# Kernel tuning notes

Hardware: AMD Instinct MI355X
Metric: run time of the kernel (lower is better)

## Reference

```python
import jax, jax.numpy as jnp
import numpy as np

H = 16  # num_heads
EPS = 1e-12  # F.normalize eps


def setup_inputs() -> dict:
    key = jax.random.key(0)
    ks = jax.random.split(key, 7)
    B, L, D = 2, 2048, 1024
    s = 0.02  # small init scale for numerical sanity
    return {
        "x": jax.random.normal(ks[0], (B, L, D), dtype=jnp.float32),
        "Wq": jax.random.normal(ks[1], (D, D), dtype=jnp.float32) * s,
        "Wk": jax.random.normal(ks[2], (D, D), dtype=jnp.float32) * s,
        "Wv": jax.random.normal(ks[3], (D, D), dtype=jnp.float32) * s,
        "Wo": jax.random.normal(ks[4], (D, D), dtype=jnp.float32) * s,
        "Wb": jax.random.normal(ks[5], (D, H), dtype=jnp.float32) * s,
        "bb": jnp.zeros((H,), dtype=jnp.float32),
    }


def _l2norm(t):
    # matches torch F.normalize(p=2, dim=-1): x / max(||x||, eps)
    n = jnp.sqrt(jnp.sum(t * t, axis=-1, keepdims=True))
    return t / jnp.maximum(n, EPS)


def reference(x, Wq, Wk, Wv, Wo, Wb, bb):
    B, L, Dm = x.shape
    Dh = Dm // H
    q = (x @ Wq).reshape(B, L, H, Dh)
    k = (x @ Wk).reshape(B, L, H, Dh)
    v = (x @ Wv).reshape(B, L, H, Dh)
    beta = jax.nn.sigmoid(x @ Wb + bb)  # [B, L, H]
    q = _l2norm(q)
    k = _l2norm(k)
    # out[b,l,h,e] = sum_{t<=l} beta[b,t,h] * <q[b,l,h], k[b,t,h]> * v[b,t,h,e]
    # Exact reformulation of the cumsum-of-outer-products in the source,
    # avoiding the B*L*H*Dh*Dh state blow-up.
    scores = jnp.einsum('blhd,bthd->bhlt', q, k)
    scores = scores * beta.transpose(0, 2, 1)[:, :, None, :]  # scale by beta_t
    mask = jnp.tril(jnp.ones((L, L), dtype=scores.dtype))  # causal incl. diagonal
    scores = scores * mask
    out = jnp.einsum('bhlt,bthe->blhe', scores, v).reshape(B, L, Dm)
    return out @ Wo
```

## Files before the change

### kernel.cpp

```cpp
#include <hip/hip_runtime.h>
#include <stdint.h>

#define DEV static __device__ __forceinline__

typedef __bf16 bf16x8 __attribute__((ext_vector_type(8)));
typedef unsigned short u16x8 __attribute__((ext_vector_type(8)));
typedef float f32x4 __attribute__((ext_vector_type(4)));

DEV unsigned short f2bf(float f) {
    unsigned int u = __builtin_bit_cast(unsigned int, f);
    u = (u + 0x7FFFu + ((u >> 16) & 1u)) >> 16;
    return (unsigned short)u;
}
DEV float bf2f(unsigned short h) {
    unsigned int u = ((unsigned int)h) << 16;
    return __builtin_bit_cast(float, u);
}

__global__ __launch_bounds__(256) void k_cvt(const float4* __restrict__ src,
                                             ushort4* __restrict__ dst, int n4) {
    int i = blockIdx.x * 256 + threadIdx.x;
    if (i < n4) {
        float4 v = src[i];
        ushort4 o;
        o.x = f2bf(v.x); o.y = f2bf(v.y); o.z = f2bf(v.z); o.w = f2bf(v.w);
        dst[i] = o;
    }
}

__global__ __launch_bounds__(256) void k_transpose_w(
    const float* __restrict__ Wq, const float* __restrict__ Wk,
    const float* __restrict__ Wv, const float* __restrict__ Wo,
    unsigned short* __restrict__ Wqkvt, unsigned short* __restrict__ Wot) {
    __shared__ float tile[32][33];
    int z = blockIdx.z;
    const float* W = (z == 0) ? Wq : (z == 1) ? Wk : (z == 2) ? Wv : Wo;
    int k0 = blockIdx.x * 32, n0 = blockIdx.y * 32;
    int tx = threadIdx.x, ty = threadIdx.y;
    #pragma unroll
    for (int r = 0; r < 32; r += 8)
        tile[ty + r][tx] = W[(size_t)(k0 + ty + r) * 1024 + n0 + tx];
    __syncthreads();
    #pragma unroll
    for (int r = 0; r < 32; r += 8) {
        float v = tile[tx][ty + r];
        int n = n0 + ty + r, k = k0 + tx;
        if (z < 3) Wqkvt[(size_t)(z * 1024 + n) * 1024 + k] = f2bf(v);
        else       Wot[(size_t)n * 1024 + k] = f2bf(v);
    }
}

__global__ __launch_bounds__(256) void k_beta(const float* __restrict__ x,
                                              const float* __restrict__ Wb,
                                              const float* __restrict__ bb,
                                              float* __restrict__ beta) {
    __shared__ float WbT[16 * 1024];
    int tid = threadIdx.x;
    #pragma unroll
    for (int j = 0; j < 16; j++) {
        int idx4 = tid + 256 * j;
        float4 v = ((const float4*)Wb)[idx4];
        int i = idx4 >> 2;
        int h0 = (idx4 & 3) * 4;
        WbT[(h0 + 0) * 1024 + (i ^ ((h0 + 0) << 2))] = v.x;
        WbT[(h0 + 1) * 1024 + (i ^ ((h0 + 1) << 2))] = v.y;
        WbT[(h0 + 2) * 1024 + (i ^ ((h0 + 2) << 2))] = v.z;
        WbT[(h0 + 3) * 1024 + (i ^ ((h0 + 3) << 2))] = v.w;
    }
    __syncthreads();
    int w = tid >> 6, lane = tid & 63;
    #pragma unroll 1
    for (int r = 0; r < 4; r++) {
        int row = blockIdx.x * 16 + w * 4 + r;
        const float* xr = x + (size_t)row * 1024;
        float acc[16] = {};
        #pragma unroll
        for (int k = 0; k < 16; k++) {
            int i = lane + 64 * k;
            float xv = xr[i];
            #pragma unroll
            for (int h = 0; h < 16; h++)
                acc[h] += xv * WbT[h * 1024 + (i ^ (h << 2))];
        }
        #pragma unroll
        for (int h = 0; h < 16; h++) {
            #pragma unroll
            for (int m = 32; m; m >>= 1) acc[h] += __shfl_xor(acc[h], m, 64);
        }
        if (lane == 0) {
            #pragma unroll
            for (int h = 0; h < 16; h++)
                beta[row * 16 + h] = 1.f / (1.f + __expf(-(acc[h] + bb[h])));
        }
    }
}

__global__ __launch_bounds__(256) void k_norm(unsigned short* __restrict__ qk,
                                              const float* __restrict__ beta) {
    int gid = blockIdx.x * 4 + (threadIdx.x >> 6);
    int lane = threadIdx.x & 63;
    int row = gid >> 4, h = gid & 15;
    unsigned short* p = qk + (size_t)row * 3072 + h * 64;
    float v = bf2f(p[lane]);
    float ss = v * v;
    #pragma unroll
    for (int m = 32; m; m >>= 1) ss += __shfl_xor(ss, m, 64);
    float scale = 1.f / fmaxf(sqrtf(ss), 1e-12f);
    if (beta) scale *= beta[row * 16 + h];
    p[lane] = f2bf(v * scale);
}

template <bool OUT_BF16>
__global__ __launch_bounds__(256) void k_gemm(const unsigned short* __restrict__ A,
                                              const unsigned short* __restrict__ Bt,
                                              void* __restrict__ C, int ldc) {
    __shared__ unsigned short As[128 * 32];
    __shared__ unsigned short Bs[128 * 32];
    int m0 = blockIdx.x * 128, n0 = blockIdx.y * 128;
    int tid = threadIdx.x;
    int w = tid >> 6, lane = tid & 63, g = lane >> 4, ln = lane & 15;
    int wr = w >> 1, wc = w & 1;
    f32x4 acc[4][4] = {};
    for (int k0 = 0; k0 < 1024; k0 += 32) {
        #pragma unroll
        for (int cc = 0; cc < 2; cc++) {
            int c = tid + cc * 256;
            int row = c >> 2, sl = c & 3;
            int ps = (sl + (row >> 1)) & 3;
            uint4 da = *(const uint4*)(A + (size_t)(m0 + row) * 1024 + k0 + sl * 8);
            *(uint4*)(&As[row * 32 + ps * 8]) = da;
            uint4 db = *(const uint4*)(Bt + (size_t)(n0 + row) * 1024 + k0 + sl * 8);
            *(uint4*)(&Bs[row * 32 + ps * 8]) = db;
        }
        __syncthreads();
        bf16x8 af[4], bfr[4];
        #pragma unroll
        for (int mi = 0; mi < 4; mi++) {
            int row = wr * 64 + mi * 16 + ln;
            int ps = (g + (row >> 1)) & 3;
            af[mi] = *(const bf16x8*)(&As[row * 32 + ps * 8]);
        }
        #pragma unroll
        for (int ni = 0; ni < 4; ni++) {
            int row = wc * 64 + ni * 16 + ln;
            int ps = (g + (row >> 1)) & 3;
            bfr[ni] = *(const bf16x8*)(&Bs[row * 32 + ps * 8]);
        }
        #pragma unroll
        for (int mi = 0; mi < 4; mi++)
            #pragma unroll
            for (int ni = 0; ni < 4; ni++)
                acc[mi][ni] = __builtin_amdgcn_mfma_f32_16x16x32_bf16(
                    af[mi], bfr[ni], acc[mi][ni], 0, 0, 0);
        __syncthreads();
    }
    #pragma unroll
    for (int mi = 0; mi < 4; mi++)
        #pragma unroll
        for (int ni = 0; ni < 4; ni++)
            #pragma unroll
            for (int r = 0; r < 4; r++) {
                int row = m0 + wr * 64 + mi * 16 + g * 4 + r;
                int col = n0 + wc * 64 + ni * 16 + ln;
                float v = acc[mi][ni][r];
                if (OUT_BF16) ((unsigned short*)C)[(size_t)row * ldc + col] = f2bf(v);
                else          ((float*)C)[(size_t)row * ldc + col] = v;
            }
}

DEV int vswz(int dh, int ks) { return (ks ^ (dh & 7) ^ ((dh >> 3) & 7)) & 7; }

__global__ __launch_bounds__(256) void k_state(const unsigned short* __restrict__ QKV,
                                               unsigned short* __restrict__ Mbuf) {
    __shared__ unsigned short Kt[64 * 64];
    __shared__ unsigned short Vt[64 * 64];
    int c = blockIdx.x, bh = blockIdx.y;
    int b = bh >> 4, h = bh & 15;
    int tid = threadIdx.x, w = tid >> 6, lane = tid & 63, g = lane >> 4, ln = lane & 15;
    int row0 = b * 2048 + c * 64;
    const unsigned short* Kg = QKV + 1024;
    const unsigned short* Vg = QKV + 2048;
    #pragma unroll
    for (int cc = 0; cc < 2; cc++) {
        int ci = tid + cc * 256;
        int r = ci >> 3, sl = ci & 7;
        uint4 kd = *(const uint4*)(Kg + (size_t)(row0 + r) * 3072 + h * 64 + sl * 8);
        uint4 vd = *(const uint4*)(Vg + (size_t)(row0 + r) * 3072 + h * 64 + sl * 8);
        union { uint4 q; unsigned short s[8]; } uk, uv;
        uk.q = kd; uv.q = vd;
        #pragma unroll
        for (int i = 0; i < 8; i++) {
            int dh = sl * 8 + i;
            int off = dh * 64 + vswz(dh, r >> 3) * 8 + (r & 7);
            Kt[off] = uk.s[i];
            Vt[off] = uv.s[i];
        }
    }
    __syncthreads();
    f32x4 macc[4] = {};
    #pragma unroll
    for (int st = 0; st < 2; st++) {
        int c0 = st * 32 + g * 4;
        int rk = w * 16 + ln;
        uint2 klo = *(const uint2*)(&Kt[rk * 64 + vswz(rk, c0 >> 3) * 8 + (c0 & 7)]);
        uint2 khi = *(const uint2*)(&Kt[rk * 64 + vswz(rk, (c0 + 16) >> 3) * 8 + (c0 & 7)]);
        uint4 kc = make_uint4(klo.x, klo.y, khi.x, khi.y);
        bf16x8 bfrag = __builtin_bit_cast(bf16x8, kc);
        #pragma unroll
        for (int mt = 0; mt < 4; mt++) {
            int rv = mt * 16 + ln;
            uint2 lo = *(const uint2*)(&Vt[rv * 64 + vswz(rv, c0 >> 3) * 8 + (c0 & 7)]);
            uint2 hi = *(const uint2*)(&Vt[rv * 64 + vswz(rv, (c0 + 16) >> 3) * 8 + (c0 & 7)]);
            uint4 comb = make_uint4(lo.x, lo.y, hi.x, hi.y);
            bf16x8 afrag = __builtin_bit_cast(bf16x8, comb);
            macc[mt] = __builtin_amdgcn_mfma_f32_16x16x32_bf16(afrag, bfrag, macc[mt], 0, 0, 0);
        }
    }
    unsigned short* Mc = Mbuf + ((size_t)bh * 32 + c) * 4096;
    #pragma unroll
    for (int mt = 0; mt < 4; mt++)
        #pragma unroll
        for (int r = 0; r < 4; r++)
            Mc[(mt * 16 + g * 4 + r) * 64 + w * 16 + ln] = f2bf(macc[mt][r]);
}

__global__ __launch_bounds__(256) void k_prefix(unsigned short* __restrict__ Mbuf) {
    int bh = blockIdx.x >> 3, slice = blockIdx.x & 7;
    int base = slice * 512 + threadIdx.x * 2;
    unsigned short* M = Mbuf + (size_t)bh * 32 * 4096 + base;
    unsigned int v[32];
    #pragma unroll
    for (int c = 0; c < 32; c++) v[c] = *(const unsigned int*)(M + (size_t)c * 4096);
    float a0 = 0.f, a1 = 0.f;
    #pragma unroll
    for (int c = 0; c < 32; c++) {
        unsigned int pack = (unsigned int)f2bf(a0) | ((unsigned int)f2bf(a1) << 16);
        *(unsigned int*)(M + (size_t)c * 4096) = pack;
        a0 += bf2f((unsigned short)(v[c] & 0xFFFF));
        a1 += bf2f((unsigned short)(v[c] >> 16));
    }
}

__global__ __launch_bounds__(256) void k_attn2(const unsigned short* __restrict__ QKV,
                                               const unsigned short* __restrict__ Sbuf,
                                               unsigned short* __restrict__ attn) {
    __shared__ unsigned short Ks[64 * 64];
    __shared__ unsigned short Vt[64 * 64];
    __shared__ unsigned short STs[64 * 64];
    int qt = blockIdx.x, bh = blockIdx.y;
    int b = bh >> 4, h = bh & 15;
    int tid = threadIdx.x, w = tid >> 6, lane = tid & 63, g = lane >> 4, ln = lane & 15;
    int rowbase = b * 2048 + qt * 64;

    const unsigned short* Qrow = QKV + (size_t)(rowbase + w * 16 + ln) * 3072 + h * 64;
    bf16x8 qf[2];
    qf[0] = *(const bf16x8*)(Qrow + g * 8);
    qf[1] = *(const bf16x8*)(Qrow + 32 + g * 8);

    const unsigned short* Kg = QKV + 1024;
    const unsigned short* Vg = QKV + 2048;
    const unsigned short* Sg = Sbuf + ((size_t)bh * 32 + qt) * 4096;

    #pragma unroll
    for (int cc = 0; cc < 2; cc++) {
        int c = tid + cc * 256;
        int r = c >> 3, sl = c & 7;
        uint4 kd = *(const uint4*)(Kg + (size_t)(rowbase + r) * 3072 + h * 64 + sl * 8);
        *(uint4*)(&Ks[r * 64 + ((sl ^ (r & 7)) * 8)]) = kd;
        uint4 sd = *(const uint4*)(Sg + r * 64 + sl * 8);
        *(uint4*)(&STs[r * 64 + ((sl ^ (r & 7)) * 8)]) = sd;
        uint4 vd = *(const uint4*)(Vg + (size_t)(rowbase + r) * 3072 + h * 64 + sl * 8);
        union { uint4 q; unsigned short s[8]; } uv; uv.q = vd;
        #pragma unroll
        for (int i = 0; i < 8; i++) {
            int dh = sl * 8 + i;
            Vt[dh * 64 + vswz(dh, r >> 3) * 8 + (r & 7)] = uv.s[i];
        }
    }
    __syncthreads();

    f32x4 oacc[4] = {};

    #pragma unroll
    for (int st = 0; st < 2; st++)
        #pragma unroll
        for (int mt2 = 0; mt2 < 4; mt2++) {
            int r = mt2 * 16 + ln;
            int ps = (st * 4 + g) ^ (r & 7);
            bf16x8 a = *(const bf16x8*)(&STs[r * 64 + ps * 8]);
            oacc[mt2] = __builtin_amdgcn_mfma_f32_16x16x32_bf16(a, qf[st], oacc[mt2], 0, 0, 0);
        }

    f32x4 s[4] = {};
    #pragma unroll
    for (int st = 0; st < 2; st++)
        #pragma unroll
        for (int mt = 0; mt < 4; mt++) {
            int r = mt * 16 + ln;
            int ps = (st * 4 + g) ^ (r & 7);
            bf16x8 a = *(const bf16x8*)(&Ks[r * 64 + ps * 8]);
            s[mt] = __builtin_amdgcn_mfma_f32_16x16x32_bf16(a, qf[st], s[mt], 0, 0, 0);
        }
    {
        int qr = w * 16 + ln;
        #pragma unroll
        for (int mt = 0; mt < 4; mt++)
            #pragma unroll
            for (int r = 0; r < 4; r++)
                if (mt * 16 + g * 4 + r > qr) s[mt][r] = 0.f;
    }
    bf16x8 pf[2];
    #pragma unroll
    for (int st = 0; st < 2; st++) {
        u16x8 t;
        #pragma unroll
        for (int r = 0; r < 4; r++) {
            t[r]     = f2bf(s[2 * st][r]);
            t[4 + r] = f2bf(s[2 * st + 1][r]);
        }
        pf[st] = __builtin_bit_cast(bf16x8, t);
    }
    #pragma unroll
    for (int st = 0; st < 2; st++)
        #pragma unroll
        for (int mt2 = 0; mt2 < 4; mt2++) {
            int rv = mt2 * 16 + ln;
            int c0 = st * 32 + g * 4;
            uint2 lo = *(const uint2*)(&Vt[rv * 64 + vswz(rv, c0 >> 3) * 8 + (c0 & 7)]);
            uint2 hi = *(const uint2*)(&Vt[rv * 64 + vswz(rv, (c0 + 16) >> 3) * 8 + (c0 & 7)]);
            uint4 comb = make_uint4(lo.x, lo.y, hi.x, hi.y);
            bf16x8 a = __builtin_bit_cast(bf16x8, comb);
            oacc[mt2] = __builtin_amdgcn_mfma_f32_16x16x32_bf16(a, pf[st], oacc[mt2], 0, 0, 0);
        }
    __syncthreads();

    {
        int qr = w * 16 + ln;
        #pragma unroll
        for (int mt2 = 0; mt2 < 4; mt2++)
            #pragma unroll
            for (int r = 0; r < 4; r++) {
                int dh = mt2 * 16 + g * 4 + r;
                Ks[qr * 64 + (dh ^ ((qr & 7) << 3))] = f2bf(oacc[mt2][r]);
            }
    }
    __syncthreads();
    #pragma unroll
    for (int cc = 0; cc < 2; cc++) {
        int c = tid + cc * 256;
        int r = c >> 3, sl = c & 7;
        uint4 d = *(const uint4*)(&Ks[r * 64 + ((sl ^ (r & 7)) * 8)]);
        *(uint4*)(attn + (size_t)(rowbase + r) * 1024 + h * 64 + sl * 8) = d;
    }
}

extern "C" void kernel_launch(void* const* d_in, const int* in_sizes, int n_in,
                              void* d_out, int out_size, void* d_ws, size_t ws_size,
                              hipStream_t stream) {
    const float* x  = (const float*)d_in[0];
    const float* Wq = (const float*)d_in[1];
    const float* Wk = (const float*)d_in[2];
    const float* Wv = (const float*)d_in[3];
    const float* Wo = (const float*)d_in[4];
    const float* Wb = (const float*)d_in[5];
    const float* bb = (const float*)d_in[6];
    float* out = (float*)d_out;

    char* ws = (char*)d_ws;
    unsigned short* xb    = (unsigned short*)(ws);
    unsigned short* Mbuf  = (unsigned short*)(ws);
    unsigned short* Wqkvt = (unsigned short*)(ws + (8ull  << 20));
    unsigned short* Wot   = (unsigned short*)(ws + (14ull << 20));
    unsigned short* QKVb  = (unsigned short*)(ws + (16ull << 20));
    float*          beta  = (float*)         (ws + (40ull << 20));
    unsigned short* attn  = (unsigned short*)(ws + (41ull << 20));

    k_cvt<<<4096, 256, 0, stream>>>((const float4*)x, (ushort4*)xb, 1048576);
    k_transpose_w<<<dim3(32, 32, 4), dim3(32, 8), 0, stream>>>(Wq, Wk, Wv, Wo, Wqkvt, Wot);
    k_beta<<<256, 256, 0, stream>>>(x, Wb, bb, beta);
    k_gemm<true><<<dim3(32, 24), 256, 0, stream>>>(xb, Wqkvt, QKVb, 3072);
    k_norm<<<16384, 256, 0, stream>>>(QKVb, nullptr);
    k_norm<<<16384, 256, 0, stream>>>(QKVb + 1024, beta);
    k_state<<<dim3(32, 32), 256, 0, stream>>>(QKVb, Mbuf);
    k_prefix<<<256, 256, 0, stream>>>(Mbuf);
    k_attn2<<<dim3(32, 32), 256, 0, stream>>>(QKVb, Mbuf, attn);
    k_gemm<false><<<dim3(32, 8), 256, 0, stream>>>(attn, Wot, out, 1024);
}
```

Before: 206.3 us.

## Fuse q/k L2-norm and beta scaling into state/attn kernels; async LDS loads in GEMM

Removes the two standalone normalization kernels. k_state and k_attn2 now compute the k norm and beta scale when they load K tiles, and the q norm is applied as a row scale on the attention output. Separately, the GEMM tile staging switches to global_load_lds direct-to-LDS transfers, with the swizzle moved to the source addresses. This saves two full passes over Q/K and register staging in the GEMM, but K normalization is now recomputed in both consumer kernels.

```diff
diff --git a/kernel.cpp b/kernel.cpp
--- a/kernel.cpp
+++ b/kernel.cpp
@@ -15,6 +15,12 @@
 DEV float bf2f(unsigned short h) {
     unsigned int u = ((unsigned int)h) << 16;
     return __builtin_bit_cast(float, u);
+}
+
+DEV void gload_lds16(const unsigned short* g, unsigned short* l) {
+    __builtin_amdgcn_global_load_lds(
+        (const __attribute__((address_space(1))) unsigned int*)g,
+        (__attribute__((address_space(3))) unsigned int*)l, 16, 0, 0);
 }
 
 __global__ __launch_bounds__(256) void k_cvt(const float4* __restrict__ src,
@@ -93,21 +99,6 @@
                 beta[row * 16 + h] = 1.f / (1.f + __expf(-(acc[h] + bb[h])));
         }
     }
-}
-
-__global__ __launch_bounds__(256) void k_norm(unsigned short* __restrict__ qk,
-                                              const float* __restrict__ beta) {
-    int gid = blockIdx.x * 4 + (threadIdx.x >> 6);
-    int lane = threadIdx.x & 63;
-    int row = gid >> 4, h = gid & 15;
-    unsigned short* p = qk + (size_t)row * 3072 + h * 64;
-    float v = bf2f(p[lane]);
-    float ss = v * v;
-    #pragma unroll
-    for (int m = 32; m; m >>= 1) ss += __shfl_xor(ss, m, 64);
-    float scale = 1.f / fmaxf(sqrtf(ss), 1e-12f);
-    if (beta) scale *= beta[row * 16 + h];
-    p[lane] = f2bf(v * scale);
 }
 
 template <bool OUT_BF16>
@@ -124,13 +115,12 @@
     for (int k0 = 0; k0 < 1024; k0 += 32) {
         #pragma unroll
         for (int cc = 0; cc < 2; cc++) {
-            int c = tid + cc * 256;
-            int row = c >> 2, sl = c & 3;
-            int ps = (sl + (row >> 1)) & 3;
-            uint4 da = *(const uint4*)(A + (size_t)(m0 + row) * 1024 + k0 + sl * 8);
-            *(uint4*)(&As[row * 32 + ps * 8]) = da;
-            uint4 db = *(const uint4*)(Bt + (size_t)(n0 + row) * 1024 + k0 + sl * 8);
-            *(uint4*)(&Bs[row * 32 + ps * 8]) = db;
+            int base = (w * 2 + cc) * 64;
+            int chunk = base + lane;
+            int row = chunk >> 2, ps = chunk & 3;
+            int sl = (ps - (row >> 1)) & 3;
+            gload_lds16(A + (size_t)(m0 + row) * 1024 + k0 + sl * 8, &As[base * 8]);
+            gload_lds16(Bt + (size_t)(n0 + row) * 1024 + k0 + sl * 8, &Bs[base * 8]);
         }
         __syncthreads();
         bf16x8 af[4], bfr[4];
@@ -171,6 +161,7 @@
 DEV int vswz(int dh, int ks) { return (ks ^ (dh & 7) ^ ((dh >> 3) & 7)) & 7; }
 
 __global__ __launch_bounds__(256) void k_state(const unsigned short* __restrict__ QKV,
+                                               const float* __restrict__ beta,
                                                unsigned short* __restrict__ Mbuf) {
     __shared__ unsigned short Kt[64 * 64];
     __shared__ unsigned short Vt[64 * 64];
@@ -188,11 +179,18 @@
         uint4 vd = *(const uint4*)(Vg + (size_t)(row0 + r) * 3072 + h * 64 + sl * 8);
         union { uint4 q; unsigned short s[8]; } uk, uv;
         uk.q = kd; uv.q = vd;
+        float ssk = 0.f;
+        #pragma unroll
+        for (int i = 0; i < 8; i++) { float v = bf2f(uk.s[i]); ssk += v * v; }
+        ssk += __shfl_xor(ssk, 1, 64);
+        ssk += __shfl_xor(ssk, 2, 64);
+        ssk += __shfl_xor(ssk, 4, 64);
+        float ksc = beta[(row0 + r) * 16 + h] / fmaxf(sqrtf(ssk), 1e-12f);
         #pragma unroll
         for (int i = 0; i < 8; i++) {
             int dh = sl * 8 + i;
             int off = dh * 64 + vswz(dh, r >> 3) * 8 + (r & 7);
-            Kt[off] = uk.s[i];
+            Kt[off] = f2bf(bf2f(uk.s[i]) * ksc);
             Vt[off] = uv.s[i];
         }
     }
@@ -243,6 +241,7 @@
 
 __global__ __launch_bounds__(256) void k_attn2(const unsigned short* __restrict__ QKV,
                                                const unsigned short* __restrict__ Sbuf,
+                                               const float* __restrict__ beta,
                                                unsigned short* __restrict__ attn) {
     __shared__ unsigned short Ks[64 * 64];
     __shared__ unsigned short Vt[64 * 64];
@@ -253,9 +252,20 @@
     int rowbase = b * 2048 + qt * 64;
 
     const unsigned short* Qrow = QKV + (size_t)(rowbase + w * 16 + ln) * 3072 + h * 64;
+    u16x8 qu0 = *(const u16x8*)(Qrow + g * 8);
+    u16x8 qu1 = *(const u16x8*)(Qrow + 32 + g * 8);
     bf16x8 qf[2];
-    qf[0] = *(const bf16x8*)(Qrow + g * 8);
-    qf[1] = *(const bf16x8*)(Qrow + 32 + g * 8);
+    qf[0] = __builtin_bit_cast(bf16x8, qu0);
+    qf[1] = __builtin_bit_cast(bf16x8, qu1);
+    float ssq = 0.f;
+    #pragma unroll
+    for (int j = 0; j < 8; j++) {
+        float v0 = bf2f(qu0[j]), v1 = bf2f(qu1[j]);
+        ssq += v0 * v0 + v1 * v1;
+    }
+    ssq += __shfl_xor(ssq, 16, 64);
+    ssq += __shfl_xor(ssq, 32, 64);
+    float qscale = 1.f / fmaxf(sqrtf(ssq), 1e-12f);
 
     const unsigned short* Kg = QKV + 1024;
     const unsigned short* Vg = QKV + 2048;
@@ -266,7 +276,17 @@
         int c = tid + cc * 256;
         int r = c >> 3, sl = c & 7;
         uint4 kd = *(const uint4*)(Kg + (size_t)(rowbase + r) * 3072 + h * 64 + sl * 8);
-        *(uint4*)(&Ks[r * 64 + ((sl ^ (r & 7)) * 8)]) = kd;
+        union { uint4 q; unsigned short s[8]; } uk; uk.q = kd;
+        float ssk = 0.f;
+        #pragma unroll
+        for (int i = 0; i < 8; i++) { float v = bf2f(uk.s[i]); ssk += v * v; }
+        ssk += __shfl_xor(ssk, 1, 64);
+        ssk += __shfl_xor(ssk, 2, 64);
+        ssk += __shfl_xor(ssk, 4, 64);
+        float ksc = beta[(rowbase + r) * 16 + h] / fmaxf(sqrtf(ssk), 1e-12f);
+        #pragma unroll
+        for (int i = 0; i < 8; i++) uk.s[i] = f2bf(bf2f(uk.s[i]) * ksc);
+        *(uint4*)(&Ks[r * 64 + ((sl ^ (r & 7)) * 8)]) = uk.q;
         uint4 sd = *(const uint4*)(Sg + r * 64 + sl * 8);
         *(uint4*)(&STs[r * 64 + ((sl ^ (r & 7)) * 8)]) = sd;
         uint4 vd = *(const uint4*)(Vg + (size_t)(rowbase + r) * 3072 + h * 64 + sl * 8);
@@ -341,7 +361,7 @@
             #pragma unroll
             for (int r = 0; r < 4; r++) {
                 int dh = mt2 * 16 + g * 4 + r;
-                Ks[qr * 64 + (dh ^ ((qr & 7) << 3))] = f2bf(oacc[mt2][r]);
+                Ks[qr * 64 + (dh ^ ((qr & 7) << 3))] = f2bf(oacc[mt2][r] * qscale);
             }
     }
     __syncthreads();
@@ -379,10 +399,8 @@
     k_transpose_w<<<dim3(32, 32, 4), dim3(32, 8), 0, stream>>>(Wq, Wk, Wv, Wo, Wqkvt, Wot);
     k_beta<<<256, 256, 0, stream>>>(x, Wb, bb, beta);
     k_gemm<true><<<dim3(32, 24), 256, 0, stream>>>(xb, Wqkvt, QKVb, 3072);
-    k_norm<<<16384, 256, 0, stream>>>(QKVb, nullptr);
-    k_norm<<<16384, 256, 0, stream>>>(QKVb + 1024, beta);
-    k_state<<<dim3(32, 32), 256, 0, stream>>>(QKVb, Mbuf);
+    k_state<<<dim3(32, 32), 256, 0, stream>>>(QKVb, beta, Mbuf);
     k_prefix<<<256, 256, 0, stream>>>(Mbuf);
-    k_attn2<<<dim3(32, 32), 256, 0, stream>>>(QKVb, Mbuf, attn);
+    k_attn2<<<dim3(32, 32), 256, 0, stream>>>(QKVb, Mbuf, beta, attn);
     k_gemm<false><<<dim3(32, 8), 256, 0, stream>>>(attn, Wot, out, 1024);
 }
```

New measurement: 183.8 us. -10.9%, faster.
